# Kernel tuning notes

Measured on AMD Instinct MI355X. Metric: run time of the kernel, lower is better.

Reference implementation:

```python
import jax, jax.numpy as jnp
import numpy as np

N = 30000      # nodes
NNZ = 480000   # edges (avg degree 16)
D_IN, D_H, D_OUT = 64, 256, 128


def spmm(rows, cols, vals, feat, n):
    # (sparse [n,n] in COO) @ feat : out[r] += vals[e] * feat[cols[e]]
    return jax.ops.segment_sum(vals[:, None] * feat[cols], rows, num_segments=n)


def graph_inception(l_feat, r_feat, rows, cols, vals, W1, b1, W2, b2):
    # hop=1, eval mode (F.dropout with training=False is identity)
    n = l_feat.shape[0]
    x0 = r_feat  # dropout(Korder_list[r][0])
    x1 = l_feat  # dropout(Korder_list[l][0])
    # network_l @ x0 and network_r (=transpose) @ x1
    l_K = spmm(rows, cols, vals, x0, n)          # [N, D]
    r_K = spmm(cols, rows, vals, x1, n)          # [N, D]
    l_re = l_K @ W1 + b1                          # weight1(l_Korder)
    r_re = r_K @ W1 + b1
    # Multiply: mm(network, a) * b then weight2 (mm result equals l_K / r_K)
    l_mul = (l_K * x1) @ W2 + b2
    r_mul = (r_K * x0) @ W2 + b2
    return l_re + l_mul, r_re + r_mul


def setup_inputs() -> dict:
    key = jax.random.key(0)
    ks = jax.random.split(key, 9)
    l_feat = jax.random.normal(ks[0], (N, D_IN), jnp.float32)
    r_feat = jax.random.normal(ks[1], (N, D_IN), jnp.float32)
    edge_rows = jax.random.randint(ks[2], (NNZ,), 0, N, jnp.int32)
    edge_cols = jax.random.randint(ks[3], (NNZ,), 0, N, jnp.int32)
    edge_vals = jax.random.uniform(ks[4], (NNZ,), jnp.float32)
    W1 = jax.random.normal(ks[5], (D_IN, D_H), jnp.float32) / np.sqrt(D_IN)
    W2 = jax.random.normal(ks[6], (D_IN, D_H), jnp.float32) / np.sqrt(D_IN)
    W3 = jax.random.normal(ks[7], (D_H, D_OUT), jnp.float32) / np.sqrt(D_H)
    W4 = jax.random.normal(ks[8], (D_H, D_OUT), jnp.float32) / np.sqrt(D_H)
    return {
        "l_feat": l_feat, "r_feat": r_feat,
        "edge_rows": edge_rows, "edge_cols": edge_cols, "edge_vals": edge_vals,
        "W1": W1, "b1": jnp.zeros((D_H,), jnp.float32),
        "W2": W2, "b2": jnp.zeros((D_H,), jnp.float32),
        "W3": W3, "b3": jnp.zeros((D_OUT,), jnp.float32),
        "W4": W4, "b4": jnp.zeros((D_OUT,), jnp.float32),
    }


def reference(l_feat, r_feat, edge_rows, edge_cols, edge_vals,
              W1, b1, W2, b2, W3, b3, W4, b4):
    a1, b1_ = graph_inception(l_feat, r_feat, edge_rows, edge_cols, edge_vals, W1, b1, W2, b2)
    y1 = jax.nn.relu(a1)
    z1 = jax.nn.relu(b1_)
    a2, _ = graph_inception(y1, z1, edge_rows, edge_cols, edge_vals, W3, b3, W4, b4)
    return jax.nn.relu(a2)  # [N, 128]
```

## Files before the change

### kernel.cpp

```cpp
#include <hip/hip_runtime.h>

#define NN    30000
#define NNZE  480000
#define NPART 8
#define PROWS (NN / NPART)

using s8 = __attribute__((ext_vector_type(8))) short;
using f4 = __attribute__((ext_vector_type(4))) float;

__device__ __forceinline__ unsigned short f2bf(float x) {
    unsigned int u = __float_as_uint(x);
    u += 0x7fff + ((u >> 16) & 1);
    return (unsigned short)(u >> 16);
}
__device__ __forceinline__ float bf2f(unsigned short h) {
    return __uint_as_float(((unsigned int)h) << 16);
}
__device__ __forceinline__ float bflo(unsigned int z) {
    return __uint_as_float(z << 16);
}
__device__ __forceinline__ float bfhi(unsigned int z) {
    return __uint_as_float(z & 0xffff0000u);
}
__device__ __forceinline__ int2 nt_pair(const int2* p) {
    long long v = __builtin_nontemporal_load((const long long*)p);
    int2 r; r.x = (int)(unsigned int)v; r.y = (int)(v >> 32); return r;
}

#define FEAT4   (NN * 64 / 4)
#define PREP_W0 (2 * FEAT4)
#define PREP_W1 (PREP_W0 + 98688)
#define PREP_Z  (PREP_W1 + 2 * NN / 4)
__global__ __launch_bounds__(256) void prep_kernel(
    const float* __restrict__ lf, const float* __restrict__ rf,
    const float* __restrict__ W1, const float* __restrict__ W2,
    const float* __restrict__ W3, const float* __restrict__ W4,
    const float* __restrict__ b1, const float* __restrict__ b2,
    const float* __restrict__ b3, const float* __restrict__ b4,
    unsigned short* __restrict__ lfb, unsigned short* __restrict__ rfb,
    unsigned short* __restrict__ Wt1, unsigned short* __restrict__ Wt2,
    float* __restrict__ bias1, float* __restrict__ bias2,
    int* __restrict__ cnt)
{
    int i = blockIdx.x * 256 + threadIdx.x;
    if (i < PREP_W0) {
        const float* src = (i < FEAT4) ? lf : rf;
        unsigned short* dst = (i < FEAT4) ? lfb : rfb;
        int j = (i < FEAT4) ? i : i - FEAT4;
        float4 v = ((const float4*)src)[j];
        ushort4 o;
        o.x = f2bf(v.x); o.y = f2bf(v.y); o.z = f2bf(v.z); o.w = f2bf(v.w);
        ((ushort4*)dst)[j] = o;
    } else if (i < PREP_W1) {
        int j = i - PREP_W0;
        if (j < 32768) {
            int n = j >> 7, k = j & 127;
            float v = (k < 64) ? W1[(size_t)k * 256 + n] : W2[(size_t)(k - 64) * 256 + n];
            Wt1[j] = f2bf(v);
        } else if (j < 32768 + 65536) {
            int q = j - 32768;
            int n = q >> 9, k = q & 511;
            float v = (k < 256) ? W3[(size_t)k * 128 + n] : W4[(size_t)(k - 256) * 128 + n];
            Wt2[q] = f2bf(v);
        } else if (j < 98304 + 256) {
            int n = j - 98304; bias1[n] = b1[n] + b2[n];
        } else if (j < 98560 + 128) {
            int n = j - 98560; bias2[n] = b3[n] + b4[n];
        }
    } else if (i < PREP_Z) {
        int j = i - PREP_W1;
        ((int4*)cnt)[j] = make_int4(0, 0, 0, 0);
    }
}

__global__ __launch_bounds__(256) void hist_part_kernel(
    const int* __restrict__ rows, const int* __restrict__ cols,
    int* __restrict__ rc, int* __restrict__ cc)
{
    int part = blockIdx.x & (NPART - 1);
    int lo = part * PROWS, hi = lo + PROWS;
    int nb = gridDim.x >> 3;
    int bj = blockIdx.x >> 3;
    int stride = nb * 256;
    for (int e = bj * 256 + threadIdx.x; e < NNZE; e += stride) {
        int r = __builtin_nontemporal_load(rows + e);
        if (r >= lo && r < hi) atomicAdd(&rc[r], 1);
        int c = __builtin_nontemporal_load(cols + e);
        if (c >= lo && c < hi) atomicAdd(&cc[c], 1);
    }
}

#define SCB 118
__global__ __launch_bounds__(256) void scan_local_kernel(
    const int* __restrict__ rc, const int* __restrict__ cc,
    int* __restrict__ rf, int* __restrict__ cf, int* __restrict__ totals)
{
    int b = blockIdx.x;
    const int* cnt = (b < SCB) ? rc : cc;
    int*       esc = (b < SCB) ? rf : cf;
    int lb = (b < SCB) ? b : b - SCB;
    int t = threadIdx.x;
    int idx = lb * 256 + t;

    __shared__ int s[256];
    int v = (idx < NN) ? cnt[idx] : 0;
    s[t] = v;
    __syncthreads();
#pragma unroll
    for (int off = 1; off < 256; off <<= 1) {
        int u = (t >= off) ? s[t - off] : 0;
        __syncthreads();
        s[t] += u;
        __syncthreads();
    }
    if (idx < NN) esc[idx] = s[t] - v;
    if (t == 255) totals[b] = s[t];
}

__global__ __launch_bounds__(128) void scan_tot_kernel(int* __restrict__ totals)
{
    int base = blockIdx.x * SCB;
    int t = threadIdx.x;
    __shared__ int s[128];
    int v = (t < SCB) ? totals[base + t] : 0;
    s[t] = v;
    __syncthreads();
#pragma unroll
    for (int off = 1; off < 128; off <<= 1) {
        int u = (t >= off) ? s[t - off] : 0;
        __syncthreads();
        s[t] += u;
        __syncthreads();
    }
    if (t < SCB) totals[base + t] = s[t] - v;
}

__global__ __launch_bounds__(256) void scan_add_kernel(
    int* __restrict__ rf, int* __restrict__ cf,
    int* __restrict__ rp, int* __restrict__ cp,
    const int* __restrict__ totals)
{
    int b = blockIdx.x;
    int lb = (b < SCB) ? b : b - SCB;
    int t = threadIdx.x;
    int idx = lb * 256 + t;
    int off = totals[b];
    if (idx < NN) {
        if (b < SCB) { int v = rf[idx] + off; rp[idx] = v; rf[idx] = v; }
        else         { int v = cf[idx] + off; cp[idx] = v; cf[idx] = v; }
    }
    if (b == 0   && t == 0) rp[NN] = NNZE;
    if (b == SCB && t == 0) cp[NN] = NNZE;
}

__global__ __launch_bounds__(256) void scatter_part_kernel(
    const int* __restrict__ rows, const int* __restrict__ cols,
    const float* __restrict__ vals,
    int* __restrict__ rf, int* __restrict__ cf,
    int2* __restrict__ csr_pair, int2* __restrict__ csc_pair)
{
    int part = blockIdx.x & (NPART - 1);
    int lo = part * PROWS, hi = lo + PROWS;
    int nb = gridDim.x >> 3;
    int bj = blockIdx.x >> 3;
    int stride = nb * 256;
    for (int e = bj * 256 + threadIdx.x; e < NNZE; e += stride) {
        int r = __builtin_nontemporal_load(rows + e);
        int c = __builtin_nontemporal_load(cols + e);
        float fv = __builtin_nontemporal_load(vals + e);
        int vb = __float_as_int(fv);
        if (r >= lo && r < hi) {
            int p = atomicAdd(&rf[r], 1);
            csr_pair[p] = make_int2(c, vb);
        }
        if (c >= lo && c < hi) {
            int q = atomicAdd(&cf[c], 1);
            csc_pair[q] = make_int2(r, vb);
        }
    }
}

__global__ __launch_bounds__(256) void gather64_x_kernel(
    const int* __restrict__ rp, const int2* __restrict__ rpair,
    const int* __restrict__ cp, const int2* __restrict__ cpair,
    const unsigned short* __restrict__ lfb, const unsigned short* __restrict__ rfb,
    unsigned short* __restrict__ X1, unsigned short* __restrict__ X2)
{
    int side = blockIdx.y;
    const int*  ptr  = side ? cp    : rp;
    const int2* pair = side ? cpair : rpair;
    const unsigned int* gf = (const unsigned int*)(side ? lfb : rfb);
    const unsigned int* mf = (const unsigned int*)(side ? rfb : lfb);
    unsigned int* X = (unsigned int*)(side ? X2 : X1);

    int w = blockIdx.x * 8 + (threadIdx.x >> 5);
    int l = threadIdx.x & 31;
    int e0 = ptr[w], e1 = ptr[w + 1];
    float a0 = 0.f, a1 = 0.f;
    int e = e0;
    for (; e + 7 < e1; e += 8) {
        int2 p[8];
#pragma unroll
        for (int j = 0; j < 8; ++j) p[j] = nt_pair(&pair[e + j]);
        unsigned int z[8];
#pragma unroll
        for (int j = 0; j < 8; ++j) z[j] = gf[(size_t)p[j].x * 32 + l];
#pragma unroll
        for (int j = 0; j < 8; ++j) {
            float v = __int_as_float(p[j].y);
            a0 += v * bflo(z[j]);
            a1 += v * bfhi(z[j]);
        }
    }
    for (; e < e1; ++e) {
        int2 p0 = nt_pair(&pair[e]);
        unsigned int z0 = gf[(size_t)p0.x * 32 + l];
        float v = __int_as_float(p0.y);
        a0 += v * bflo(z0);
        a1 += v * bfhi(z0);
    }
    unsigned int m = mf[(size_t)w * 32 + l];
    float m0 = a0 * bflo(m);
    float m1 = a1 * bfhi(m);
    X[(size_t)w * 64 + l]      = (unsigned int)f2bf(a0) | ((unsigned int)f2bf(a1) << 16);
    X[(size_t)w * 64 + 32 + l] = (unsigned int)f2bf(m0) | ((unsigned int)f2bf(m1) << 16);
}

__global__ __launch_bounds__(256) void gather256_x_kernel(
    const int* __restrict__ ptr, const int2* __restrict__ pair,
    const unsigned short* __restrict__ z1b, const unsigned short* __restrict__ y1b,
    unsigned short* __restrict__ X3)
{
    int w    = blockIdx.x * 4 + (threadIdx.x >> 6);
    int lane = threadIdx.x & 63;
    int e0 = ptr[w], e1 = ptr[w + 1];
    const ushort4* Z = (const ushort4*)z1b;
    f4 acc = {0.f, 0.f, 0.f, 0.f};
    int e = e0;
    for (; e + 7 < e1; e += 8) {
        int2 p[8];
#pragma unroll
        for (int j = 0; j < 8; ++j) p[j] = nt_pair(&pair[e + j]);
        ushort4 z[8];
#pragma unroll
        for (int j = 0; j < 8; ++j) z[j] = Z[(size_t)p[j].x * 64 + lane];
#pragma unroll
        for (int j = 0; j < 8; ++j) {
            float v = __int_as_float(p[j].y);
            acc[0] += v * bf2f(z[j].x);
            acc[1] += v * bf2f(z[j].y);
            acc[2] += v * bf2f(z[j].z);
            acc[3] += v * bf2f(z[j].w);
        }
    }
    for (; e < e1; ++e) {
        int2 p0 = nt_pair(&pair[e]);
        float v0 = __int_as_float(p0.y);
        ushort4 z0 = Z[(size_t)p0.x * 64 + lane];
        acc[0] += v0 * bf2f(z0.x);
        acc[1] += v0 * bf2f(z0.y);
        acc[2] += v0 * bf2f(z0.z);
        acc[3] += v0 * bf2f(z0.w);
    }
    ushort4 y = ((const ushort4*)y1b)[(size_t)w * 64 + lane];
    ushort4 o0, o1;
    o0.x = f2bf(acc[0]); o0.y = f2bf(acc[1]); o0.z = f2bf(acc[2]); o0.w = f2bf(acc[3]);
    o1.x = f2bf(acc[0] * bf2f(y.x));
    o1.y = f2bf(acc[1] * bf2f(y.y));
    o1.z = f2bf(acc[2] * bf2f(y.z));
    o1.w = f2bf(acc[3] * bf2f(y.w));
    ((ushort4*)X3)[(size_t)w * 128 + lane]      = o0;
    ((ushort4*)X3)[(size_t)w * 128 + 64 + lane] = o1;
}

template<int K, int DOUT, bool OUT_BF16>
__global__ __launch_bounds__(256) void mfma_gemm_kernel(
    const unsigned short* Xa, const unsigned short* Xb,
    const unsigned short* __restrict__ Wt, const float* __restrict__ bias,
    void* outa, void* outb)
{
    constexpr int WC = DOUT / 4;
    constexpr int FN = WC / 16;
    __shared__ s8 sX[64 * 8];
    __shared__ s8 sW[DOUT * 8];

    const unsigned short* X = blockIdx.y ? Xb : Xa;
    void* outv              = blockIdx.y ? outb : outa;

    const int t       = threadIdx.x;
    const int rowbase = blockIdx.x * 64;
    const int wid     = t >> 6;
    const int lane    = t & 63;
    const int l15     = lane & 15;
    const int kg      = lane >> 4;

    f4 acc[4][FN] = {};

    for (int kc = 0; kc < K; kc += 64) {
#pragma unroll
        for (int it = 0; it < 2; ++it) {
            int ch = t + it * 256;
            int r = ch >> 3, c = ch & 7;
            int row = rowbase + r;
            s8 v = {};
            if (row < NN) v = ((const s8*)X)[((size_t)row * K + kc) / 8 + c];
            sX[(r << 3) | (c ^ (r & 7))] = v;
        }
#pragma unroll
        for (int it = 0; it < DOUT / 32; ++it) {
            int ch = t + it * 256;
            int n = ch >> 3, c = ch & 7;
            sW[(n << 3) | (c ^ (n & 7))] = ((const s8*)Wt)[((size_t)n * K + kc) / 8 + c];
        }
        __syncthreads();

#pragma unroll
        for (int ks = 0; ks < 2; ++ks) {
            int cch = ks * 4 + kg;
            s8 a[4], b[FN];
#pragma unroll
            for (int fm = 0; fm < 4; ++fm) {
                int r0 = fm * 16 + l15;
                a[fm] = sX[(r0 << 3) | (cch ^ (r0 & 7))];
            }
#pragma unroll
            for (int fn = 0; fn < FN; ++fn) {
                int n0 = wid * WC + fn * 16 + l15;
                b[fn] = sW[(n0 << 3) | (cch ^ (n0 & 7))];
            }
#pragma unroll
            for (int fm = 0; fm < 4; ++fm)
#pragma unroll
                for (int fn = 0; fn < FN; ++fn)
                    acc[fm][fn] = __builtin_amdgcn_mfma_f32_16x16x32_bf16(
                        a[fm], b[fn], acc[fm][fn], 0, 0, 0);
        }
        __syncthreads();
    }

#pragma unroll
    for (int fm = 0; fm < 4; ++fm) {
#pragma unroll
        for (int fn = 0; fn < FN; ++fn) {
            int col = wid * WC + fn * 16 + l15;
            float bv = bias[col];
#pragma unroll
            for (int j = 0; j < 4; ++j) {
                int row = rowbase + fm * 16 + kg * 4 + j;
                if (row < NN) {
                    float v = fmaxf(acc[fm][fn][j] + bv, 0.f);
                    if constexpr (OUT_BF16)
                        ((unsigned short*)outv)[(size_t)row * DOUT + col] = f2bf(v);
                    else
                        ((float*)outv)[(size_t)row * DOUT + col] = v;
                }
            }
        }
    }
}

extern "C" void kernel_launch(void* const* d_in, const int* in_sizes, int n_in,
                              void* d_out, int out_size, void* d_ws, size_t ws_size,
                              hipStream_t stream)
{
    const float* l_feat = (const float*)d_in[0];
    const float* r_feat = (const float*)d_in[1];
    const int*   rows   = (const int*)  d_in[2];
    const int*   cols   = (const int*)  d_in[3];
    const float* vals   = (const float*)d_in[4];
    const float* W1     = (const float*)d_in[5];
    const float* b1     = (const float*)d_in[6];
    const float* W2     = (const float*)d_in[7];
    const float* b2     = (const float*)d_in[8];
    const float* W3     = (const float*)d_in[9];
    const float* b3     = (const float*)d_in[10];
    const float* W4     = (const float*)d_in[11];
    const float* b4     = (const float*)d_in[12];
    float* out = (float*)d_out;

    char* p = (char*)d_ws;
    unsigned short* X1  = (unsigned short*)p; p += (size_t)NN * 128 * 2;
    unsigned short* X2  = (unsigned short*)p; p += (size_t)NN * 128 * 2;
    unsigned short* X3  = (unsigned short*)p; p += (size_t)NN * 512 * 2;
    unsigned short* z1b = (unsigned short*)p; p += (size_t)NN * 256 * 2;
    unsigned short* y1b = (unsigned short*)p; p += (size_t)NN * 256 * 2;
    unsigned short* lfb = (unsigned short*)p; p += (size_t)NN * 64 * 2;
    unsigned short* rfb = (unsigned short*)p; p += (size_t)NN * 64 * 2;
    int* row_cnt  = (int*)p; p += (size_t)NN * 4;
    int* col_cnt  = (int*)p; p += (size_t)NN * 4;
    int* row_fill = (int*)p; p += (size_t)NN * 4;
    int* col_fill = (int*)p; p += (size_t)NN * 4;
    int* totals   = (int*)p; p += 256 * 4;
    unsigned short* Wt1 = (unsigned short*)p; p += 32768 * 2;
    unsigned short* Wt2 = (unsigned short*)p; p += 65536 * 2;
    float* bias1 = (float*)p; p += 256 * 4;
    float* bias2 = (float*)p; p += 128 * 4;
    int*   row_ptr  = (int*)p; p += (size_t)(NN + 4) * 4;
    int*   col_ptr  = (int*)p; p += (size_t)(NN + 4) * 4;
    int2*  csr_pair = (int2*)p; p += (size_t)NNZE * 8;
    int2*  csc_pair = (int2*)p; p += (size_t)NNZE * 8;

    prep_kernel<<<(PREP_Z + 255) / 256, 256, 0, stream>>>(
        l_feat, r_feat, W1, W2, W3, W4, b1, b2, b3, b4,
        lfb, rfb, Wt1, Wt2, bias1, bias2, row_cnt);

    hist_part_kernel<<<1024, 256, 0, stream>>>(rows, cols, row_cnt, col_cnt);

    scan_local_kernel<<<2 * SCB, 256, 0, stream>>>(row_cnt, col_cnt, row_fill, col_fill, totals);
    scan_tot_kernel<<<2, 128, 0, stream>>>(totals);
    scan_add_kernel<<<2 * SCB, 256, 0, stream>>>(row_fill, col_fill, row_ptr, col_ptr, totals);

    scatter_part_kernel<<<1024, 256, 0, stream>>>(
        rows, cols, vals, row_fill, col_fill, csr_pair, csc_pair);

    {
        dim3 grid(NN / 8, 2);
        gather64_x_kernel<<<grid, 256, 0, stream>>>(
            row_ptr, csr_pair, col_ptr, csc_pair, lfb, rfb, X1, X2);
    }

    {
        dim3 grid((NN + 63) / 64, 2);
        mfma_gemm_kernel<128, 256, true><<<grid, 256, 0, stream>>>(
            X1, X2, Wt1, bias1, y1b, z1b);
    }

    gather256_x_kernel<<<NN / 4, 256, 0, stream>>>(row_ptr, csr_pair, z1b, y1b, X3);

    {
        dim3 grid((NN + 63) / 64, 1);
        mfma_gemm_kernel<512, 128, false><<<grid, 256, 0, stream>>>(
            X3, X3, Wt2, bias2, out, out);
    }
}
```

Measured before the change: 211.2 us.

## Record per-edge ranks in histogram to remove scatter atomics and fuse scan passes

The histogram kernel now stores each edge's atomicAdd return value as its rank within its row and column. The scatter then computes output positions as the row/column pointer plus that rank, so it no longer needs atomics on separate fill arrays. The histogram drops its partitioned loop and reads each edge once. The total-scan and add-offset kernels are merged into one, with each block redoing the small scan of the 118 block totals, which removes a launch. In exchange it adds 3.84 MB of rank writes and reads, and the order of edges within a row becomes the atomic order from the histogram kernel.

Measured after the change: 199.7 us. 1.06x faster.

```diff
diff --git a/kernel.cpp b/kernel.cpp
--- a/kernel.cpp
+++ b/kernel.cpp
@@ -73,31 +73,28 @@
     }
 }
 
-__global__ __launch_bounds__(256) void hist_part_kernel(
+__global__ __launch_bounds__(256) void histrank_kernel(
     const int* __restrict__ rows, const int* __restrict__ cols,
-    int* __restrict__ rc, int* __restrict__ cc)
-{
-    int part = blockIdx.x & (NPART - 1);
-    int lo = part * PROWS, hi = lo + PROWS;
-    int nb = gridDim.x >> 3;
-    int bj = blockIdx.x >> 3;
-    int stride = nb * 256;
-    for (int e = bj * 256 + threadIdx.x; e < NNZE; e += stride) {
+    int* __restrict__ rc, int* __restrict__ cc,
+    int* __restrict__ rank_r, int* __restrict__ rank_c)
+{
+    int e = blockIdx.x * 256 + threadIdx.x;
+    if (e < NNZE) {
         int r = __builtin_nontemporal_load(rows + e);
-        if (r >= lo && r < hi) atomicAdd(&rc[r], 1);
+        rank_r[e] = atomicAdd(&rc[r], 1);
         int c = __builtin_nontemporal_load(cols + e);
-        if (c >= lo && c < hi) atomicAdd(&cc[c], 1);
+        rank_c[e] = atomicAdd(&cc[c], 1);
     }
 }
 
 #define SCB 118
 __global__ __launch_bounds__(256) void scan_local_kernel(
     const int* __restrict__ rc, const int* __restrict__ cc,
-    int* __restrict__ rf, int* __restrict__ cf, int* __restrict__ totals)
+    int* __restrict__ rp, int* __restrict__ cp, int* __restrict__ totals)
 {
     int b = blockIdx.x;
     const int* cnt = (b < SCB) ? rc : cc;
-    int*       esc = (b < SCB) ? rf : cf;
+    int*       esc = (b < SCB) ? rp : cp;
     int lb = (b < SCB) ? b : b - SCB;
     int t = threadIdx.x;
     int idx = lb * 256 + t;
@@ -117,46 +114,38 @@
     if (t == 255) totals[b] = s[t];
 }
 
-__global__ __launch_bounds__(128) void scan_tot_kernel(int* __restrict__ totals)
-{
-    int base = blockIdx.x * SCB;
+__global__ __launch_bounds__(256) void scan_addtot_kernel(
+    int* __restrict__ rp, int* __restrict__ cp, const int* __restrict__ totals)
+{
+    int b = blockIdx.x;
+    int side = (b >= SCB) ? 1 : 0;
+    int lb = side ? b - SCB : b;
     int t = threadIdx.x;
+
     __shared__ int s[128];
-    int v = (t < SCB) ? totals[base + t] : 0;
-    s[t] = v;
+    if (t < 128) s[t] = (t < SCB) ? totals[side * SCB + t] : 0;
     __syncthreads();
 #pragma unroll
     for (int off = 1; off < 128; off <<= 1) {
-        int u = (t >= off) ? s[t - off] : 0;
-        __syncthreads();
-        s[t] += u;
-        __syncthreads();
-    }
-    if (t < SCB) totals[base + t] = s[t] - v;
-}
-
-__global__ __launch_bounds__(256) void scan_add_kernel(
-    int* __restrict__ rf, int* __restrict__ cf,
-    int* __restrict__ rp, int* __restrict__ cp,
-    const int* __restrict__ totals)
-{
-    int b = blockIdx.x;
-    int lb = (b < SCB) ? b : b - SCB;
-    int t = threadIdx.x;
+        int u = 0;
+        if (t < 128 && t >= off) u = s[t - off];
+        __syncthreads();
+        if (t < 128) s[t] += u;
+        __syncthreads();
+    }
+    int off = (lb == 0) ? 0 : s[lb - 1];
     int idx = lb * 256 + t;
-    int off = totals[b];
-    if (idx < NN) {
-        if (b < SCB) { int v = rf[idx] + off; rp[idx] = v; rf[idx] = v; }
-        else         { int v = cf[idx] + off; cp[idx] = v; cf[idx] = v; }
-    }
+    int* ptr = side ? cp : rp;
+    if (idx < NN) ptr[idx] += off;
     if (b == 0   && t == 0) rp[NN] = NNZE;
     if (b == SCB && t == 0) cp[NN] = NNZE;
 }
 
-__global__ __launch_bounds__(256) void scatter_part_kernel(
+__global__ __launch_bounds__(256) void scatter_rank_kernel(
     const int* __restrict__ rows, const int* __restrict__ cols,
     const float* __restrict__ vals,
-    int* __restrict__ rf, int* __restrict__ cf,
+    const int* __restrict__ rank_r, const int* __restrict__ rank_c,
+    const int* __restrict__ rp, const int* __restrict__ cp,
     int2* __restrict__ csr_pair, int2* __restrict__ csc_pair)
 {
     int part = blockIdx.x & (NPART - 1);
@@ -170,11 +159,11 @@
         float fv = __builtin_nontemporal_load(vals + e);
         int vb = __float_as_int(fv);
         if (r >= lo && r < hi) {
-            int p = atomicAdd(&rf[r], 1);
+            int p = rp[r] + __builtin_nontemporal_load(rank_r + e);
             csr_pair[p] = make_int2(c, vb);
         }
         if (c >= lo && c < hi) {
-            int q = atomicAdd(&cf[c], 1);
+            int q = cp[c] + __builtin_nontemporal_load(rank_c + e);
             csc_pair[q] = make_int2(r, vb);
         }
     }
@@ -388,8 +377,6 @@
     unsigned short* rfb = (unsigned short*)p; p += (size_t)NN * 64 * 2;
     int* row_cnt  = (int*)p; p += (size_t)NN * 4;
     int* col_cnt  = (int*)p; p += (size_t)NN * 4;
-    int* row_fill = (int*)p; p += (size_t)NN * 4;
-    int* col_fill = (int*)p; p += (size_t)NN * 4;
     int* totals   = (int*)p; p += 256 * 4;
     unsigned short* Wt1 = (unsigned short*)p; p += 32768 * 2;
     unsigned short* Wt2 = (unsigned short*)p; p += 65536 * 2;
@@ -399,19 +386,21 @@
     int*   col_ptr  = (int*)p; p += (size_t)(NN + 4) * 4;
     int2*  csr_pair = (int2*)p; p += (size_t)NNZE * 8;
     int2*  csc_pair = (int2*)p; p += (size_t)NNZE * 8;
+    int*   rank_r   = (int*)p; p += (size_t)NNZE * 4;
+    int*   rank_c   = (int*)p; p += (size_t)NNZE * 4;
 
     prep_kernel<<<(PREP_Z + 255) / 256, 256, 0, stream>>>(
         l_feat, r_feat, W1, W2, W3, W4, b1, b2, b3, b4,
         lfb, rfb, Wt1, Wt2, bias1, bias2, row_cnt);
 
-    hist_part_kernel<<<1024, 256, 0, stream>>>(rows, cols, row_cnt, col_cnt);
-
-    scan_local_kernel<<<2 * SCB, 256, 0, stream>>>(row_cnt, col_cnt, row_fill, col_fill, totals);
-    scan_tot_kernel<<<2, 128, 0, stream>>>(totals);
-    scan_add_kernel<<<2 * SCB, 256, 0, stream>>>(row_fill, col_fill, row_ptr, col_ptr, totals);
-
-    scatter_part_kernel<<<1024, 256, 0, stream>>>(
-        rows, cols, vals, row_fill, col_fill, csr_pair, csc_pair);
+    histrank_kernel<<<(NNZE + 255) / 256, 256, 0, stream>>>(
+        rows, cols, row_cnt, col_cnt, rank_r, rank_c);
+
+    scan_local_kernel<<<2 * SCB, 256, 0, stream>>>(row_cnt, col_cnt, row_ptr, col_ptr, totals);
+    scan_addtot_kernel<<<2 * SCB, 256, 0, stream>>>(row_ptr, col_ptr, totals);
+
+    scatter_rank_kernel<<<1024, 256, 0, stream>>>(
+        rows, cols, vals, rank_r, rank_c, row_ptr, col_ptr, csr_pair, csc_pair);
 
     {
         dim3 grid(NN / 8, 2);
```
